# Performance work log

Measured on AMD Instinct MI355X. Metric: run time of the kernel, lower is better.

The kernel has to match this reference:

```python
import jax, jax.numpy as jnp
import numpy as np

BS, RES = 2, 512
H_LVL = RES // 2 + 1   # floor(512/2)+1 = 257
W_LVL = RES            # 512
NQ = H_LVL * W_LVL     # 131584
D, HEADS, PTS = 128, 8, 4
DH = D // HEADS


def setup_inputs() -> dict:
    key = jax.random.key(0)
    ks = jax.random.split(key, 9)
    s = 0.02  # weight init scale
    return {
        "query":   jax.random.normal(ks[0], (BS, NQ, D), jnp.float32),
        "W_value": jax.random.normal(ks[1], (D, D), jnp.float32) * s,
        "b_value": jax.random.normal(ks[2], (D,), jnp.float32) * s,
        "W_off":   jax.random.normal(ks[3], (D, HEADS * PTS * 2), jnp.float32) * s,
        "b_off":   jax.random.normal(ks[4], (HEADS * PTS * 2,), jnp.float32) * s,
        "W_attn":  jax.random.normal(ks[5], (D, HEADS * PTS), jnp.float32) * s,
        "b_attn":  jax.random.normal(ks[6], (HEADS * PTS,), jnp.float32) * s,
        "W_out":   jax.random.normal(ks[7], (D, D), jnp.float32) * s,
        "b_out":   jax.random.normal(ks[8], (D,), jnp.float32) * s,
    }


def _bilinear_zeros(V, x, y, H, W):
    """grid_sample(mode=bilinear, padding=zeros, align_corners=False) equivalent.
    V: [G, H*W, DH]; x, y: [G, S] pixel coords. Returns [G, S, DH]."""
    x0 = jnp.floor(x); y0 = jnp.floor(y)
    x0i = x0.astype(jnp.int32); y0i = y0.astype(jnp.int32)
    x1i = x0i + 1; y1i = y0i + 1
    wx1 = x - x0; wx0 = 1.0 - wx1
    wy1 = y - y0; wy0 = 1.0 - wy1

    def corner(xi, yi, w):
        valid = (xi >= 0) & (xi < W) & (yi >= 0) & (yi < H)
        idx = jnp.clip(yi, 0, H - 1) * W + jnp.clip(xi, 0, W - 1)
        val = jnp.take_along_axis(V, idx[:, :, None], axis=1)  # [G,S,DH]
        return (w * valid.astype(w.dtype))[:, :, None] * val

    return (corner(x0i, y0i, wx0 * wy0) + corner(x1i, y0i, wx1 * wy0)
            + corner(x0i, y1i, wx0 * wy1) + corner(x1i, y1i, wx1 * wy1))


def reference(query, W_value, b_value, W_off, b_off, W_attn, b_attn, W_out, b_out):
    B, NQ_, D_ = query.shape
    H, W = H_LVL, W_LVL

    # projections (mmcv MSDeformAttn)
    value = (query @ W_value + b_value).reshape(B, NQ_, HEADS, DH)
    offsets = (query @ W_off + b_off).reshape(B, NQ_, HEADS, PTS, 2)  # num_levels=1
    attn = jax.nn.softmax((query @ W_attn + b_attn).reshape(B, NQ_, HEADS, PTS), axis=-1)

    # reference points: meshgrid of normalized (col=x, row=y), row-major flatten
    gy, gx = jnp.meshgrid(jnp.linspace(0.0, 1.0, H), jnp.linspace(0.0, 1.0, W), indexing="ij")
    ref = jnp.stack([gx, gy], axis=-1).reshape(NQ_, 2).astype(query.dtype)  # [NQ,2]

    # sampling locations in [0,1]; offset normalizer = (W, H)
    norm = jnp.array([W, H], dtype=query.dtype)
    loc = ref[None, :, None, None, :] + offsets / norm  # [B,NQ,HEADS,PTS,2]

    # grid_sample align_corners=False: pixel = loc*size - 0.5
    x = loc[..., 0] * W - 0.5
    y = loc[..., 1] * H - 0.5

    G = B * HEADS
    V = value.transpose(0, 2, 1, 3).reshape(G, H * W, DH)          # [G,HW,DH]
    xs = x.transpose(0, 2, 1, 3).reshape(G, NQ_ * PTS)
    ys = y.transpose(0, 2, 1, 3).reshape(G, NQ_ * PTS)

    samp = _bilinear_zeros(V, xs, ys, H, W).reshape(B, HEADS, NQ_, PTS, DH)
    aw = attn.transpose(0, 2, 1, 3)                                 # [B,HEADS,NQ,PTS]
    out = jnp.einsum("bhqp,bhqpd->bqhd", aw, samp).reshape(B, NQ_, D_)
    out = out @ W_out + b_out

    # mmcv adds identity inside the attention module; outer forward adds residual again
    return out + query + query
```

## Files before the change

kernel.cpp:

```cpp
#include <hip/hip_runtime.h>
#include <hip/hip_bf16.h>

#define BS     2
#define H_LVL  257
#define W_LVL  512
#define NQC    (H_LVL * W_LVL)
#define DD     128
#define HEADS  8
#define PTS    4
#define DH     16
#define MTOT   (BS * NQC)

typedef float v4f __attribute__((ext_vector_type(4)));
typedef short v8s __attribute__((ext_vector_type(8)));

static __device__ __forceinline__ unsigned short f2bb(float f) {
    union { float f; unsigned int u; } v; v.f = f;
    const unsigned int u = v.u;
    return (unsigned short)((u + 0x7fffu + ((u >> 16) & 1u)) >> 16);
}
static __device__ __forceinline__ float bb2f(unsigned short h) {
    union { unsigned int u; float f; } v; v.u = ((unsigned int)h) << 16;
    return v.f;
}
static __device__ __forceinline__ void fma4(float4& acc, float w, const unsigned short* p) {
    const ushort4 r = *(const ushort4*)p;
    acc.x = fmaf(w, bb2f(r.x), acc.x);
    acc.y = fmaf(w, bb2f(r.y), acc.y);
    acc.z = fmaf(w, bb2f(r.z), acc.z);
    acc.w = fmaf(w, bb2f(r.w), acc.w);
}

__global__ __launch_bounds__(256) void prep_kernel(
    const float* __restrict__ Wv, const float* __restrict__ bv,
    const float* __restrict__ Woff, const float* __restrict__ boff,
    const float* __restrict__ Wattn, const float* __restrict__ battn,
    const float* __restrict__ Wout,
    unsigned short* __restrict__ Wt224, unsigned short* __restrict__ WtO,
    float* __restrict__ bcat224)
{
    const int id = blockIdx.x * 256 + threadIdx.x;
    {
        const int n = id >> 7, k = id & 127;
        float v;
        if (n < 128)      v = Wv[k * DD + n];
        else if (n < 192) v = Woff[k * 64 + (n - 128)];
        else              v = Wattn[k * 32 + (n - 192)];
        Wt224[id] = f2bb(v);
    }
    if (id < 128 * 128) {
        const int n = id >> 7, k = id & 127;
        WtO[id] = f2bb(Wout[k * DD + n]);
    }
    if (id < 224)
        bcat224[id] = (id < 128) ? bv[id] : (id < 192 ? boff[id - 128] : battn[id - 192]);
}

__global__ __launch_bounds__(256) void gemm_fused_kernel(
    const float* __restrict__ A,
    const unsigned short* __restrict__ Wt,
    const float* __restrict__ bias,
    unsigned short* __restrict__ value,
    unsigned short* __restrict__ proj)
{
    constexpr int NT = 14;
    constexpr int NC = NT * 16;
    __shared__ unsigned short As[64 * 136];
    __shared__ unsigned short Ws[NC * 136];
    const int t = threadIdx.x;
    const long long m0 = (long long)blockIdx.x * 64;

    {
        const float4* src = (const float4*)(A + m0 * DD);
        #pragma unroll
        for (int rep = 0; rep < 8; ++rep) {
            const int c = rep * 256 + t;
            const int m = c >> 5, f4 = c & 31;
            const float4 v = src[c];
            ushort4 hq;
            hq.x = f2bb(v.x); hq.y = f2bb(v.y); hq.z = f2bb(v.z); hq.w = f2bb(v.w);
            *(ushort4*)(&As[m * 136 + f4 * 4]) = hq;
        }
    }
    {
        const uint4* src = (const uint4*)Wt;
        #pragma unroll
        for (int rep = 0; rep < 14; ++rep) {
            const int c = rep * 256 + t;
            const int n = c >> 4, kc = c & 15;
            *(uint4*)(&Ws[n * 136 + kc * 8]) = src[c];
        }
    }
    __syncthreads();

    const int lane = t & 63, wave = t >> 6;
    const int l15 = lane & 15, quad = lane >> 4;

    v4f acc[NT];
    #pragma unroll
    for (int nt = 0; nt < NT; ++nt) { v4f z = {0.f, 0.f, 0.f, 0.f}; acc[nt] = z; }

    const int arow = wave * 16 + l15;
    #pragma unroll
    for (int kk = 0; kk < 4; ++kk) {
        const v8s a = *(const v8s*)(&As[arow * 136 + kk * 32 + quad * 8]);
        #pragma unroll
        for (int nt = 0; nt < NT; ++nt) {
            const v8s b = *(const v8s*)(&Ws[(nt * 16 + l15) * 136 + kk * 32 + quad * 8]);
            acc[nt] = __builtin_amdgcn_mfma_f32_16x16x32_bf16(a, b, acc[nt], 0, 0, 0);
        }
    }

    const long long mbase = m0 + wave * 16 + quad * 4;
    const int b = (int)(m0 / NQC);
    #pragma unroll
    for (int nt = 0; nt < 8; ++nt) {
        const float bi = bias[nt * 16 + l15];
        #pragma unroll
        for (int r = 0; r < 4; ++r) {
            const long long q = (mbase + r) - (long long)b * NQC;
            value[((long long)(b * HEADS + nt) * NQC + q) * DH + l15] =
                f2bb(acc[nt][r] + bi);
        }
    }
    #pragma unroll
    for (int nt = 8; nt < 14; ++nt) {
        const float bi = bias[nt * 16 + l15];
        #pragma unroll
        for (int r = 0; r < 4; ++r)
            proj[(mbase + r) * 96 + (nt - 8) * 16 + l15] = f2bb(acc[nt][r] + bi);
    }
}

template<int NT, int MODE>
__global__ __launch_bounds__(256) void gemm_kernel(
    const float* __restrict__ A,
    const unsigned short* __restrict__ Wt,
    const float* __restrict__ bias,
    unsigned short* __restrict__ dst_bf,
    float* __restrict__ dst_f,
    const float* __restrict__ query)
{
    constexpr int NC = NT * 16;
    __shared__ unsigned short As[64 * 136];
    __shared__ unsigned short Ws[NC * 136];
    const int t = threadIdx.x;
    const long long m0 = (long long)blockIdx.x * 64;

    {
        const float4* src = (const float4*)(A + m0 * DD);
        #pragma unroll
        for (int rep = 0; rep < 8; ++rep) {
            const int c = rep * 256 + t;
            const int m = c >> 5, f4 = c & 31;
            const float4 v = src[c];
            ushort4 hq;
            hq.x = f2bb(v.x); hq.y = f2bb(v.y); hq.z = f2bb(v.z); hq.w = f2bb(v.w);
            *(ushort4*)(&As[m * 136 + f4 * 4]) = hq;
        }
    }
    {
        const uint4* src = (const uint4*)Wt;
        for (int c = t; c < NC * 16; c += 256) {
            const int n = c >> 4, kc = c & 15;
            *(uint4*)(&Ws[n * 136 + kc * 8]) = src[c];
        }
    }
    __syncthreads();

    const int lane = t & 63, wave = t >> 6;
    const int l15 = lane & 15, quad = lane >> 4;

    v4f acc[NT];
    #pragma unroll
    for (int nt = 0; nt < NT; ++nt) { v4f z = {0.f, 0.f, 0.f, 0.f}; acc[nt] = z; }

    const int arow = wave * 16 + l15;
    #pragma unroll
    for (int kk = 0; kk < 4; ++kk) {
        const v8s a = *(const v8s*)(&As[arow * 136 + kk * 32 + quad * 8]);
        #pragma unroll
        for (int nt = 0; nt < NT; ++nt) {
            const v8s b = *(const v8s*)(&Ws[(nt * 16 + l15) * 136 + kk * 32 + quad * 8]);
            acc[nt] = __builtin_amdgcn_mfma_f32_16x16x32_bf16(a, b, acc[nt], 0, 0, 0);
        }
    }

    const long long mbase = m0 + wave * 16 + quad * 4;
    if (MODE == 0) {
        const int b = (int)(m0 / NQC);
        #pragma unroll
        for (int nt = 0; nt < NT; ++nt) {
            const float bi = bias[nt * 16 + l15];
            #pragma unroll
            for (int r = 0; r < 4; ++r) {
                const long long q = (mbase + r) - (long long)b * NQC;
                dst_bf[((long long)(b * HEADS + nt) * NQC + q) * DH + l15] =
                    f2bb(acc[nt][r] + bi);
            }
        }
    } else {
        #pragma unroll
        for (int nt = 0; nt < NT; ++nt) {
            const float bi = bias[nt * 16 + l15];
            #pragma unroll
            for (int r = 0; r < 4; ++r) {
                const long long idx = (mbase + r) * DD + nt * 16 + l15;
                dst_f[idx] = acc[nt][r] + bi + 2.0f * query[idx];
            }
        }
    }
}

__global__ __launch_bounds__(256) void sample_out_kernel(
    const unsigned short* __restrict__ proj,
    const unsigned short* __restrict__ value,
    const unsigned short* __restrict__ WtO,
    const float* __restrict__ bout,
    const float* __restrict__ query,
    float* __restrict__ out)
{
    __shared__ union {
        float projF[64][96];
        unsigned short Ws[128 * 136];
    } sh;
    __shared__ unsigned short As[64 * 136];

    const int t = threadIdx.x;
    const long long qbase = (long long)blockIdx.x * 64;

    {
        const ushort4* src = (const ushort4*)(proj + qbase * 96);
        #pragma unroll
        for (int rep = 0; rep < 6; ++rep) {
            const int i = rep * 256 + t;
            const ushort4 r = src[i];
            const int qq = (i * 4) / 96, c = (i * 4) % 96;
            sh.projF[qq][c]     = bb2f(r.x);
            sh.projF[qq][c + 1] = bb2f(r.y);
            sh.projF[qq][c + 2] = bb2f(r.z);
            sh.projF[qq][c + 3] = bb2f(r.w);
        }
    }
    __syncthreads();

    const int b = (int)(qbase / NQC);
    const int lq = t & 31;
    const int h = lq >> 2, p_own = lq & 3;
    const int lbase = (t & 63) & ~3;
    const unsigned short* V = value + (size_t)(b * HEADS + h) * NQC * DH + p_own * 4;

    #pragma unroll
    for (int it = 0; it < 8; ++it) {
        const int q_loc = it * 8 + (t >> 5);
        const int qidx = (int)(qbase - (long long)b * NQC) + q_loc;
        const int row = qidx >> 9, col = qidx & 511;

        const float offx = sh.projF[q_loc][(h * PTS + p_own) * 2];
        const float offy = sh.projF[q_loc][(h * PTS + p_own) * 2 + 1];
        const float al   = sh.projF[q_loc][64 + h * PTS + p_own];
        float mx = fmaxf(al, __shfl_xor(al, 1));
        mx = fmaxf(mx, __shfl_xor(mx, 2));
        const float e = __expf(al - mx);
        float sm = e + __shfl_xor(e, 1);
        sm += __shfl_xor(sm, 2);
        const float aw = e / sm;

        const float x = (float)col * (1.0f / 511.0f) * (float)W_LVL + offx - 0.5f;
        const float y = (float)row * (1.0f / 256.0f) * (float)H_LVL + offy - 0.5f;
        const float x0f = floorf(x), y0f = floorf(y);
        const int x0 = (int)x0f, y0 = (int)y0f;
        const int x1 = x0 + 1, y1 = y0 + 1;
        const float wx1 = x - x0f, wx0 = 1.0f - wx1;
        const float wy1 = y - y0f, wy0 = 1.0f - wy1;
        const float vx0 = (x0 >= 0 && x0 < W_LVL) ? 1.f : 0.f;
        const float vx1 = (x1 >= 0 && x1 < W_LVL) ? 1.f : 0.f;
        const float vy0 = (y0 >= 0 && y0 < H_LVL) ? 1.f : 0.f;
        const float vy1 = (y1 >= 0 && y1 < H_LVL) ? 1.f : 0.f;
        float w00 = aw * wx0 * wy0 * vx0 * vy0;
        float w01 = aw * wx1 * wy0 * vx1 * vy0;
        float w10 = aw * wx0 * wy1 * vx0 * vy1;
        float w11 = aw * wx1 * wy1 * vx1 * vy1;
        const int xc0 = min(max(x0, 0), W_LVL - 1), xc1 = min(max(x1, 0), W_LVL - 1);
        const int yc0 = min(max(y0, 0), H_LVL - 1), yc1 = min(max(y1, 0), H_LVL - 1);
        int i00 = yc0 * W_LVL + xc0, i01 = yc0 * W_LVL + xc1;
        int i10 = yc1 * W_LVL + xc0, i11 = yc1 * W_LVL + xc1;

        float4 acc = {0.f, 0.f, 0.f, 0.f};
        #pragma unroll
        for (int p = 0; p < 4; ++p) {
            const int src = lbase + p;
            const float W00 = __shfl(w00, src, 64), W01 = __shfl(w01, src, 64);
            const float W10 = __shfl(w10, src, 64), W11 = __shfl(w11, src, 64);
            const int   I00 = __shfl(i00, src, 64), I01 = __shfl(i01, src, 64);
            const int   I10 = __shfl(i10, src, 64), I11 = __shfl(i11, src, 64);
            fma4(acc, W00, V + (size_t)I00 * DH);
            fma4(acc, W01, V + (size_t)I01 * DH);
            fma4(acc, W10, V + (size_t)I10 * DH);
            fma4(acc, W11, V + (size_t)I11 * DH);
        }
        ushort4 h4;
        h4.x = f2bb(acc.x); h4.y = f2bb(acc.y); h4.z = f2bb(acc.z); h4.w = f2bb(acc.w);
        *(ushort4*)(&As[q_loc * 136 + h * 16 + p_own * 4]) = h4;
    }
    __syncthreads();

    {
        const uint4* src = (const uint4*)WtO;
        #pragma unroll
        for (int rep = 0; rep < 8; ++rep) {
            const int c = rep * 256 + t;
            const int n = c >> 4, kc = c & 15;
            *(uint4*)(&sh.Ws[n * 136 + kc * 8]) = src[c];
        }
    }
    __syncthreads();

    const int lane = t & 63, wave = t >> 6;
    const int l15 = lane & 15, quad = lane >> 4;

    v4f acc[8];
    #pragma unroll
    for (int nt = 0; nt < 8; ++nt) { v4f z = {0.f, 0.f, 0.f, 0.f}; acc[nt] = z; }

    const int arow = wave * 16 + l15;
    #pragma unroll
    for (int kk = 0; kk < 4; ++kk) {
        const v8s a = *(const v8s*)(&As[arow * 136 + kk * 32 + quad * 8]);
        #pragma unroll
        for (int nt = 0; nt < 8; ++nt) {
            const v8s bfr = *(const v8s*)(&sh.Ws[(nt * 16 + l15) * 136 + kk * 32 + quad * 8]);
            acc[nt] = __builtin_amdgcn_mfma_f32_16x16x32_bf16(a, bfr, acc[nt], 0, 0, 0);
        }
    }

    const long long mbase = qbase + wave * 16 + quad * 4;
    #pragma unroll
    for (int nt = 0; nt < 8; ++nt) {
        const float bi = bout[nt * 16 + l15];
        #pragma unroll
        for (int r = 0; r < 4; ++r) {
            const long long idx = (mbase + r) * DD + nt * 16 + l15;
            out[idx] = acc[nt][r] + bi + 2.0f * query[idx];
        }
    }
}

__global__ __launch_bounds__(256) void sample2_fb_kernel(
    const float* __restrict__ query,
    const float* __restrict__ Woff, const float* __restrict__ boff,
    const float* __restrict__ Wattn, const float* __restrict__ battn,
    const unsigned short* __restrict__ value,
    float* __restrict__ attn_out)
{
    __shared__ float projF[8][96];
    const int t = threadIdx.x;
    const long long qbase = (long long)blockIdx.x * 8;

    __shared__ float qs[8][DD];
    {
        const int qi = t >> 5, k4 = (t & 31) * 4;
        const float4 v = *(const float4*)(query + (qbase + qi) * DD + k4);
        qs[qi][k4] = v.x; qs[qi][k4 + 1] = v.y; qs[qi][k4 + 2] = v.z; qs[qi][k4 + 3] = v.w;
    }
    __syncthreads();
    for (int task = t; task < 768; task += 256) {
        const int qi = task / 96, c = task % 96;
        float a; const float* wp; int stride;
        if (c < 64) { a = boff[c];       wp = Woff  + c;        stride = 64; }
        else        { a = battn[c - 64]; wp = Wattn + (c - 64); stride = 32; }
        for (int k = 0; k < DD; ++k) a += qs[qi][k] * wp[k * stride];
        projF[qi][c] = a;
    }
    __syncthreads();

    const int q_loc = t >> 5, lq = t & 31;
    const int h = lq >> 2, p_own = lq & 3;
    const long long bq = qbase + q_loc;
    const int b = (int)(bq / NQC);
    const int qidx = (int)(bq - (long long)b * NQC);
    const int row = qidx >> 9, col = qidx & 511;

    const float offx = projF[q_loc][(h * PTS + p_own) * 2];
    const float offy = projF[q_loc][(h * PTS + p_own) * 2 + 1];
    const float al   = projF[q_loc][64 + h * PTS + p_own];
    float mx = fmaxf(al, __shfl_xor(al, 1));
    mx = fmaxf(mx, __shfl_xor(mx, 2));
    const float e = __expf(al - mx);
    float sm = e + __shfl_xor(e, 1);
    sm += __shfl_xor(sm, 2);
    const float aw = e / sm;

    const float x = (float)col * (1.0f / 511.0f) * (float)W_LVL + offx - 0.5f;
    const float y = (float)row * (1.0f / 256.0f) * (float)H_LVL + offy - 0.5f;
    const float x0f = floorf(x), y0f = floorf(y);
    const int x0 = (int)x0f, y0 = (int)y0f;
    const int x1 = x0 + 1, y1 = y0 + 1;
    const float wx1 = x - x0f, wx0 = 1.0f - wx1;
    const float wy1 = y - y0f, wy0 = 1.0f - wy1;
    const float vx0 = (x0 >= 0 && x0 < W_LVL) ? 1.f : 0.f;
    const float vx1 = (x1 >= 0 && x1 < W_LVL) ? 1.f : 0.f;
    const float vy0 = (y0 >= 0 && y0 < H_LVL) ? 1.f : 0.f;
    const float vy1 = (y1 >= 0 && y1 < H_LVL) ? 1.f : 0.f;
    float w00 = aw * wx0 * wy0 * vx0 * vy0;
    float w01 = aw * wx1 * wy0 * vx1 * vy0;
    float w10 = aw * wx0 * wy1 * vx0 * vy1;
    float w11 = aw * wx1 * wy1 * vx1 * vy1;
    const int xc0 = min(max(x0, 0), W_LVL - 1), xc1 = min(max(x1, 0), W_LVL - 1);
    const int yc0 = min(max(y0, 0), H_LVL - 1), yc1 = min(max(y1, 0), H_LVL - 1);
    int i00 = yc0 * W_LVL + xc0, i01 = yc0 * W_LVL + xc1;
    int i10 = yc1 * W_LVL + xc0, i11 = yc1 * W_LVL + xc1;

    const int dq4 = p_own;
    const unsigned short* V = value + (size_t)(b * HEADS + h) * NQC * DH + dq4 * 4;
    float4 acc = {0.f, 0.f, 0.f, 0.f};
    const int lbase = (t & 63) & ~3;
    #pragma unroll
    for (int p = 0; p < 4; ++p) {
        const int src = lbase + p;
        const float W00 = __shfl(w00, src, 64), W01 = __shfl(w01, src, 64);
        const float W10 = __shfl(w10, src, 64), W11 = __shfl(w11, src, 64);
        const int   I00 = __shfl(i00, src, 64), I01 = __shfl(i01, src, 64);
        const int   I10 = __shfl(i10, src, 64), I11 = __shfl(i11, src, 64);
        fma4(acc, W00, V + (size_t)I00 * DH);
        fma4(acc, W01, V + (size_t)I01 * DH);
        fma4(acc, W10, V + (size_t)I10 * DH);
        fma4(acc, W11, V + (size_t)I11 * DH);
    }
    *(float4*)(attn_out + bq * DD + h * DH + dq4 * 4) = acc;
}

extern "C" void kernel_launch(void* const* d_in, const int* in_sizes, int n_in,
                              void* d_out, int out_size, void* d_ws, size_t ws_size,
                              hipStream_t stream) {
    const float* query = (const float*)d_in[0];
    const float* Wv    = (const float*)d_in[1];
    const float* bv    = (const float*)d_in[2];
    const float* Woff  = (const float*)d_in[3];
    const float* boff  = (const float*)d_in[4];
    const float* Wattn = (const float*)d_in[5];
    const float* battn = (const float*)d_in[6];
    const float* Wout  = (const float*)d_in[7];
    const float* bout  = (const float*)d_in[8];
    float* out = (float*)d_out;

    char* ws = (char*)d_ws;
    size_t off = 0;
    unsigned short* Wt224 = (unsigned short*)(ws + off); off += 224 * 128 * 2;
    unsigned short* WtO   = (unsigned short*)(ws + off); off += 128 * 128 * 2;
    float*          bcat  = (float*)(ws + off);          off += 224 * 4;
    off = (off + 255) & ~(size_t)255;
    unsigned short* value = (unsigned short*)(ws + off);
    off += (size_t)BS * HEADS * NQC * DH * 2;
    off = (off + 255) & ~(size_t)255;
    unsigned short* proj = (unsigned short*)(ws + off);
    const size_t proj_need = (size_t)MTOT * 96 * 2;
    const bool precomp = (ws_size >= off + proj_need);

    prep_kernel<<<112, 256, 0, stream>>>(Wv, bv, Woff, boff, Wattn, battn, Wout,
                                         Wt224, WtO, bcat);
    if (precomp) {
        gemm_fused_kernel<<<MTOT / 64, 256, 0, stream>>>(query, Wt224, bcat, value, proj);
        sample_out_kernel<<<MTOT / 64, 256, 0, stream>>>(proj, value, WtO, bout, query, out);
    } else {
        gemm_kernel<8, 0><<<MTOT / 64, 256, 0, stream>>>(query, Wt224, bcat, value,
                                                         nullptr, nullptr);
        sample2_fb_kernel<<<MTOT / 8, 256, 0, stream>>>(query, Woff, boff,
                                                        Wattn, battn, value, out);
        gemm_kernel<8, 2><<<MTOT / 64, 256, 0, stream>>>(out, WtO, bout, nullptr, out, query);
    }
}
```

Baseline: 398.9 us.

## Pre-swizzle output weights into MFMA fragment order and shrink LDS usage

```diff
diff --git a/kernel.cpp b/kernel.cpp
--- a/kernel.cpp
+++ b/kernel.cpp
@@ -37,7 +37,7 @@
     const float* __restrict__ Wattn, const float* __restrict__ battn,
     const float* __restrict__ Wout,
     unsigned short* __restrict__ Wt224, unsigned short* __restrict__ WtO,
-    float* __restrict__ bcat224)
+    unsigned short* __restrict__ WtOf, float* __restrict__ bcat224)
 {
     const int id = blockIdx.x * 256 + threadIdx.x;
     {
@@ -51,6 +51,12 @@
     if (id < 128 * 128) {
         const int n = id >> 7, k = id & 127;
         WtO[id] = f2bb(Wout[k * DD + n]);
+    }
+    if (id < 128 * 128) {
+        const int j = id & 7, l = (id >> 3) & 63, nt = (id >> 9) & 7, kk = id >> 12;
+        const int n = nt * 16 + (l & 15);
+        const int k = kk * 32 + (l >> 4) * 8 + j;
+        WtOf[id] = f2bb(Wout[k * DD + n]);
     }
     if (id < 224)
         bcat224[id] = (id < 128) ? bv[id] : (id < 192 ? boff[id - 128] : battn[id - 192]);
@@ -215,31 +221,23 @@
 __global__ __launch_bounds__(256) void sample_out_kernel(
     const unsigned short* __restrict__ proj,
     const unsigned short* __restrict__ value,
-    const unsigned short* __restrict__ WtO,
+    const unsigned short* __restrict__ WtOf,
     const float* __restrict__ bout,
     const float* __restrict__ query,
     float* __restrict__ out)
 {
-    __shared__ union {
-        float projF[64][96];
-        unsigned short Ws[128 * 136];
-    } sh;
+    __shared__ unsigned short projS[64 * 96];
     __shared__ unsigned short As[64 * 136];
 
     const int t = threadIdx.x;
     const long long qbase = (long long)blockIdx.x * 64;
 
     {
-        const ushort4* src = (const ushort4*)(proj + qbase * 96);
-        #pragma unroll
-        for (int rep = 0; rep < 6; ++rep) {
+        const uint4* src = (const uint4*)(proj + qbase * 96);
+        #pragma unroll
+        for (int rep = 0; rep < 3; ++rep) {
             const int i = rep * 256 + t;
-            const ushort4 r = src[i];
-            const int qq = (i * 4) / 96, c = (i * 4) % 96;
-            sh.projF[qq][c]     = bb2f(r.x);
-            sh.projF[qq][c + 1] = bb2f(r.y);
-            sh.projF[qq][c + 2] = bb2f(r.z);
-            sh.projF[qq][c + 3] = bb2f(r.w);
+            *(uint4*)(&projS[i * 8]) = src[i];
         }
     }
     __syncthreads();
@@ -256,9 +254,9 @@
         const int qidx = (int)(qbase - (long long)b * NQC) + q_loc;
         const int row = qidx >> 9, col = qidx & 511;
 
-        const float offx = sh.projF[q_loc][(h * PTS + p_own) * 2];
-        const float offy = sh.projF[q_loc][(h * PTS + p_own) * 2 + 1];
-        const float al   = sh.projF[q_loc][64 + h * PTS + p_own];
+        const float offx = bb2f(projS[q_loc * 96 + lq * 2]);
+        const float offy = bb2f(projS[q_loc * 96 + lq * 2 + 1]);
+        const float al   = bb2f(projS[q_loc * 96 + 64 + lq]);
         float mx = fmaxf(al, __shfl_xor(al, 1));
         mx = fmaxf(mx, __shfl_xor(mx, 2));
         const float e = __expf(al - mx);
@@ -301,18 +299,7 @@
         }
         ushort4 h4;
         h4.x = f2bb(acc.x); h4.y = f2bb(acc.y); h4.z = f2bb(acc.z); h4.w = f2bb(acc.w);
-        *(ushort4*)(&As[q_loc * 136 + h * 16 + p_own * 4]) = h4;
-    }
-    __syncthreads();
-
-    {
-        const uint4* src = (const uint4*)WtO;
-        #pragma unroll
-        for (int rep = 0; rep < 8; ++rep) {
-            const int c = rep * 256 + t;
-            const int n = c >> 4, kc = c & 15;
-            *(uint4*)(&sh.Ws[n * 136 + kc * 8]) = src[c];
-        }
+        *(ushort4*)(&As[q_loc * 136 + lq * 4]) = h4;
     }
     __syncthreads();
 
@@ -329,7 +316,7 @@
         const v8s a = *(const v8s*)(&As[arow * 136 + kk * 32 + quad * 8]);
         #pragma unroll
         for (int nt = 0; nt < 8; ++nt) {
-            const v8s bfr = *(const v8s*)(&sh.Ws[(nt * 16 + l15) * 136 + kk * 32 + quad * 8]);
+            const v8s bfr = *(const v8s*)(WtOf + (size_t)((kk * 8 + nt) * 64 + lane) * 8);
             acc[nt] = __builtin_amdgcn_mfma_f32_16x16x32_bf16(a, bfr, acc[nt], 0, 0, 0);
         }
     }
@@ -448,6 +435,7 @@
     size_t off = 0;
     unsigned short* Wt224 = (unsigned short*)(ws + off); off += 224 * 128 * 2;
     unsigned short* WtO   = (unsigned short*)(ws + off); off += 128 * 128 * 2;
+    unsigned short* WtOf  = (unsigned short*)(ws + off); off += 128 * 128 * 2;
     float*          bcat  = (float*)(ws + off);          off += 224 * 4;
     off = (off + 255) & ~(size_t)255;
     unsigned short* value = (unsigned short*)(ws + off);
@@ -458,10 +446,10 @@
     const bool precomp = (ws_size >= off + proj_need);
 
     prep_kernel<<<112, 256, 0, stream>>>(Wv, bv, Woff, boff, Wattn, battn, Wout,
-                                         Wt224, WtO, bcat);
+                                         Wt224, WtO, WtOf, bcat);
     if (precomp) {
         gemm_fused_kernel<<<MTOT / 64, 256, 0, stream>>>(query, Wt224, bcat, value, proj);
-        sample_out_kernel<<<MTOT / 64, 256, 0, stream>>>(proj, value, WtO, bout, query, out);
+        sample_out_kernel<<<MTOT / 64, 256, 0, stream>>>(proj, value, WtOf, bout, query, out);
     } else {
         gemm_kernel<8, 0><<<MTOT / 64, 256, 0, stream>>>(query, Wt224, bcat, value,
                                                          nullptr, nullptr);
```

Result: faster. 381.6 us (-4.3%).
